# Kernel optimization log

Hardware: AMD Instinct MI355X
Metric: run time of the kernel (lower is better)

Reference implementation:

```python
import jax, jax.numpy as jnp
import numpy as np

N_ENT = 100000
N_REL = 500
IN_DIM = 128
OUT_DIM = 128
N_TRIP = 250000
BN_EPS = 1e-5
LRELU_SLOPE = 0.01


def setup_inputs() -> dict:
    key = jax.random.key(0)
    ks = jax.random.split(key, 10)
    heads = jax.random.randint(ks[0], (N_TRIP, 1), 0, N_ENT, dtype=jnp.int32)
    tails = jax.random.randint(ks[1], (N_TRIP, 1), 0, N_ENT, dtype=jnp.int32)
    rels = jax.random.randint(ks[2], (N_TRIP, 1), 0, N_REL, dtype=jnp.int32)
    triplets = jnp.concatenate([heads, tails, rels], axis=1)
    embed_range = (6.0 + 2.0) / OUT_DIM  # (margin + epsilon) / out_dim
    ent_embed = jax.random.uniform(ks[3], (N_ENT, IN_DIM), jnp.float32, -embed_range, embed_range)
    rel_embed = jax.random.uniform(ks[4], (N_REL, IN_DIM), jnp.float32, -embed_range, embed_range)
    a_w = jax.random.normal(ks[5], (OUT_DIM, 3 * IN_DIM), jnp.float32) * (1.414 * (2.0 / (3 * IN_DIM + OUT_DIM)) ** 0.5)
    a_b = jnp.zeros((OUT_DIM,), jnp.float32)
    a2_w = jax.random.normal(ks[6], (1, OUT_DIM), jnp.float32) * (1.414 * (2.0 / (OUT_DIM + 1)) ** 0.5)
    a2_b = jnp.zeros((1,), jnp.float32)
    return dict(
        triplets=triplets,
        ent_embed=ent_embed,
        rel_embed=rel_embed,
        a_w=a_w,
        a_b=a_b,
        a2_w=a2_w,
        a2_b=a2_b,
        bn0_g=jnp.ones((3 * IN_DIM,), jnp.float32),
        bn0_b=jnp.zeros((3 * IN_DIM,), jnp.float32),
        bn1_g=jnp.ones((OUT_DIM,), jnp.float32),
        bn1_b=jnp.zeros((OUT_DIM,), jnp.float32),
    )


def _batchnorm(x, gamma, beta):
    # training-mode BN: batch statistics over axis 0, biased variance
    mean = jnp.mean(x, axis=0)
    var = jnp.mean(jnp.square(x - mean), axis=0)
    return (x - mean) * jax.lax.rsqrt(var + BN_EPS) * gamma + beta


def _leaky_relu(x):
    return jnp.where(x >= 0, x, LRELU_SLOPE * x)


def reference(triplets, ent_embed, rel_embed, a_w, a_b, a2_w, a2_b,
              bn0_g, bn0_b, bn1_g, bn1_b):
    t0, t1, t2 = triplets[:, 0], triplets[:, 1], triplets[:, 2]
    e0 = ent_embed[t0]           # [n, in_dim]
    e1 = ent_embed[t1]           # [n, in_dim]
    r = rel_embed[t2]            # [n, in_dim]
    h_fwd = jnp.concatenate([e0, e1, r], axis=1)    # [n, 3*in_dim]
    h_bwd = jnp.concatenate([e1, e0, -r], axis=1)   # [n, 3*in_dim]
    h = jnp.concatenate([h_fwd, h_bwd], axis=0)     # [2n, 3*in_dim]
    h = _batchnorm(h, bn0_g, bn0_b)                 # dropout omitted (eval)
    c = _batchnorm(h @ a_w.T + a_b, bn1_g, bn1_b)   # [2n, out_dim]
    b = -_leaky_relu(c @ a2_w.T + a2_b)             # [2n, 1]
    e_b = jnp.exp(b)                                # [2n, 1]

    # edges[0] = cat(t0, t1); scatter-add messages into source node slots
    seg = jnp.concatenate([t0, t1], axis=0)         # [2n]
    temp1 = e_b * c                                 # [2n, out_dim]
    ebs = jax.ops.segment_sum(e_b, seg, num_segments=N_ENT)    # [N, 1]
    hs = jax.ops.segment_sum(temp1, seg, num_segments=N_ENT)   # [N, out_dim]
    ebs = jnp.where(ebs == 0, 1e-12, ebs)
    h_ent = hs / ebs                                # [N, out_dim]

    # scatter-mean of forward-direction messages by relation id
    rel_sum = jax.ops.segment_sum(temp1[:N_TRIP], t2, num_segments=N_REL)
    rel_cnt = jax.ops.segment_sum(jnp.ones((N_TRIP, 1), temp1.dtype), t2, num_segments=N_REL)
    h_rel = rel_sum / jnp.maximum(rel_cnt, 1.0)     # [R, out_dim]
    return h_ent, h_rel
```

## Files before the change

### kernel.cpp

```cpp
#include <hip/hip_runtime.h>
#include <hip/hip_bf16.h>

#define NE 100000
#define NR 500
#define DD 128
#define NT 250000
#define NEV 500000
#define RELOFF 12800000
#define TWO_NF 500000.0f
#define NTF 250000.0f
#define TBH 2048
#define NBH ((NT + TBH - 1)/TBH)
#define NBS ((NE + 1023)/1024)

typedef __attribute__((ext_vector_type(8))) short short8;
typedef __attribute__((ext_vector_type(4))) float f32x4;

__device__ __forceinline__ float bf2f(unsigned short u){
  unsigned int x = ((unsigned int)u) << 16;
  return __uint_as_float(x);
}
__device__ __forceinline__ float bf2f_lo(unsigned int u){ return __uint_as_float(u << 16); }
__device__ __forceinline__ float bf2f_hi(unsigned int u){ return __uint_as_float(u & 0xFFFF0000u); }
__device__ __forceinline__ unsigned short f2bf(float f){
  __hip_bfloat16 h = __float2bfloat16(f);
  return *reinterpret_cast<unsigned short*>(&h);
}
__device__ __forceinline__ void atomAddF(float* p, float v){ unsafeAtomicAdd(p, v); }
__device__ __forceinline__ float wredsum(float x){
  x += __shfl_xor(x, 1, 64);  x += __shfl_xor(x, 2, 64);  x += __shfl_xor(x, 4, 64);
  x += __shfl_xor(x, 8, 64);  x += __shfl_xor(x, 16, 64); x += __shfl_xor(x, 32, 64);
  return x;
}

__global__ __launch_bounds__(256) void k_hist(const int* __restrict__ trip,
                                              int* __restrict__ cnt, int* __restrict__ gHist){
  __shared__ int h[NR];
  int t = threadIdx.x;
  for (int r = t; r < NR; r += 256) h[r] = 0;
  __syncthreads();
  int b0 = blockIdx.x*TBH, b1 = min(b0+TBH, NT);
  for (int i = b0 + t; i < b1; i += 256){
    int t0 = trip[3*i], t1 = trip[3*i+1], t2 = trip[3*i+2];
    atomicAdd(&cnt[t0], 1);
    atomicAdd(&cnt[t1], 1);
    atomicAdd(&h[t2], 1);
  }
  __syncthreads();
  for (int r = t; r < NR; r += 256) gHist[blockIdx.x*NR + r] = h[r];
}

__global__ __launch_bounds__(512) void k_histscan(const int* __restrict__ gHist,
                                                  int* __restrict__ base, int* __restrict__ cntR,
                                                  int* __restrict__ offR){
  __shared__ int sm[512];
  int r = threadIdx.x;
  int s = 0;
  if (r < NR){
    for (int b = 0; b < NBH; ++b){ base[b*NR + r] = s; s += gHist[b*NR + r]; }
    cntR[r] = s;
  }
  sm[r] = (r < NR) ? s : 0;
  __syncthreads();
  for (int st = 1; st < 512; st <<= 1){
    int x = (r >= st) ? sm[r-st] : 0;
    __syncthreads();
    sm[r] += x;
    __syncthreads();
  }
  if (r < NR){
    int off = sm[r] - s;
    offR[r] = off;
    for (int b = 0; b < NBH; ++b) base[b*NR + r] += off;
  }
  if (r == 0) offR[NR] = NT;
}

__global__ __launch_bounds__(1024) void k_scan1(const int* __restrict__ cnt,
                                                int* __restrict__ off, int* __restrict__ bsum){
  __shared__ int wsum[16];
  int t = threadIdx.x, lane = t & 63, w = t >> 6;
  int i = blockIdx.x*1024 + t;
  int v = (i < NE) ? cnt[i] : 0;
  int x = v;
  #pragma unroll
  for (int s = 1; s < 64; s <<= 1){ int y = __shfl_up(x, s, 64); if (lane >= s) x += y; }
  if (lane == 63) wsum[w] = x;
  __syncthreads();
  if (w == 0 && lane < 16){
    int xs = wsum[lane];
    #pragma unroll
    for (int s = 1; s < 16; s <<= 1){ int y = __shfl_up(xs, s, 16); if ((lane & 15) >= s) xs += y; }
    wsum[lane] = xs;
  }
  __syncthreads();
  int wprev = (w == 0) ? 0 : wsum[w-1];
  int incl = wprev + x;
  if (i < NE) off[i] = incl - v;
  if (t == 1023) bsum[blockIdx.x] = incl;
}

__global__ __launch_bounds__(128) void k_scan2(const int* __restrict__ bsum,
                                               int* __restrict__ bbase, int* __restrict__ off){
  __shared__ int sm[128];
  int t = threadIdx.x;
  int v = (t < NBS) ? bsum[t] : 0;
  sm[t] = v; __syncthreads();
  for (int s = 1; s < 128; s <<= 1){
    int x = (t >= s) ? sm[t-s] : 0;
    __syncthreads();
    sm[t] += x;
    __syncthreads();
  }
  int incl = sm[t];
  if (t < NBS) bbase[t] = incl - v;
  if (t == NBS-1) off[NE] = incl;
}

__global__ __launch_bounds__(1024) void k_scan3(int* __restrict__ off, int* __restrict__ cur,
                                                const int* __restrict__ bbase){
  int i = blockIdx.x*1024 + threadIdx.x;
  if (i < NE){
    int o = off[i] + bbase[blockIdx.x];
    off[i] = o;
    cur[i] = o;
  }
}

__global__ void k_scat_ent(const int* __restrict__ trip, int* __restrict__ curE,
                           unsigned long long* __restrict__ evE){
  int i = blockIdx.x*blockDim.x + threadIdx.x;
  if (i < NT){
    int t0 = trip[3*i+0], t1 = trip[3*i+1], t2 = trip[3*i+2];
    int p0 = atomicAdd(&curE[t0], 1);
    unsigned long long e0 = (unsigned)t0 |
      ((unsigned long long)(((unsigned)t1 << 10) | ((unsigned)t2 << 1)) << 32);
    __builtin_nontemporal_store(e0, &evE[p0]);
    int p1 = atomicAdd(&curE[t1], 1);
    unsigned long long e1 = (unsigned)t1 |
      ((unsigned long long)(((unsigned)t0 << 10) | ((unsigned)t2 << 1) | 1u) << 32);
    __builtin_nontemporal_store(e1, &evE[p1]);
  }
}

__global__ __launch_bounds__(256) void k_scat_rel(const int* __restrict__ trip,
                                                  const int* __restrict__ base,
                                                  unsigned long long* __restrict__ evR){
  __shared__ int cur[NR];
  int t = threadIdx.x;
  for (int r = t; r < NR; r += 256) cur[r] = base[blockIdx.x*NR + r];
  __syncthreads();
  int b0 = blockIdx.x*TBH, b1 = min(b0+TBH, NT);
  for (int i = b0 + t; i < b1; i += 256){
    int t0 = trip[3*i], t1 = trip[3*i+1], t2 = trip[3*i+2];
    int p = atomicAdd(&cur[t2], 1);
    unsigned long long e = (unsigned)t0 | ((unsigned long long)(unsigned)t1 << 32);
    __builtin_nontemporal_store(e, &evR[p]);
  }
}

__global__ __launch_bounds__(256) void k_entstats(const float* __restrict__ ent, const int* __restrict__ cnt,
                                                  float* __restrict__ S, float* __restrict__ Q,
                                                  unsigned short* __restrict__ Xbf){
  int j = threadIdx.x & 127;
  int half = threadIdx.x >> 7;
  int r0 = blockIdx.x*128 + half;
  int r1 = min(blockIdx.x*128 + 128, NE);
  float s = 0.f, q = 0.f;
  for (int r = r0; r < r1; r += 2){
    float x = ent[(size_t)r*DD + j];
    Xbf[(size_t)r*DD + j] = f2bf(x);
    int w = cnt[r];
    if (w){
      float wf = (float)w;
      s += wf*x; q += wf*x*x;
    }
  }
  __shared__ float ss[256], qq[256];
  ss[threadIdx.x] = s; qq[threadIdx.x] = q; __syncthreads();
  if (half == 0){
    atomAddF(&S[j], ss[j] + ss[j+128]);
    atomAddF(&Q[j], qq[j] + qq[j+128]);
  }
}

__global__ void k_alpha(const float* __restrict__ rel, const int* __restrict__ cntR,
                        const float* __restrict__ S, const float* __restrict__ Q,
                        const float* __restrict__ bn0g, const float* __restrict__ bn0b,
                        float* __restrict__ alpha0, float* __restrict__ alpha1, float* __restrict__ alpha2,
                        float* __restrict__ beta0, float* __restrict__ beta1){
  int j = threadIdx.x;
  float qr = 0.f;
  for (int k = 0; k < NR; ++k){
    float w = (float)cntR[k];
    float x = rel[k*DD + j];
    qr += w*x*x;
  }
  float mean = S[j] / TWO_NF;
  float var  = Q[j] / TWO_NF - mean*mean;
  float inv  = rsqrtf(var + 1e-5f);
  float a0 = inv * bn0g[j];
  float a1 = inv * bn0g[128+j];
  alpha0[j] = a0; alpha1[j] = a1;
  beta0[j] = bn0b[j]     - mean*a0;
  beta1[j] = bn0b[128+j] - mean*a1;
  float varR = qr / NTF;
  alpha2[j] = rsqrtf(varR + 1e-5f) * bn0g[256+j];
}

__global__ void k_bias(const float* __restrict__ aw, const float* __restrict__ ab,
                       const float* __restrict__ bn0b,
                       const float* __restrict__ beta0, const float* __restrict__ beta1,
                       float* __restrict__ bias){
  int o = blockIdx.x, j = threadIdx.x;
  const float* r = aw + (size_t)o*384;
  float p = r[j]*beta0[j] + r[128+j]*beta1[j] + r[256+j]*bn0b[256+j];
  __shared__ float sm[128];
  sm[j] = p; __syncthreads();
  for (int s = 64; s > 0; s >>= 1){ if (j < s) sm[j] += sm[j+s]; __syncthreads(); }
  if (j == 0) bias[o] = ab[o] + sm[0];
}

__global__ void k_v(const float* __restrict__ rel, const float* __restrict__ aw,
                    const float* __restrict__ alpha2, float* __restrict__ V){
  int k = blockIdx.x, o = threadIdx.x;
  __shared__ float rl[128];
  rl[o] = rel[k*DD + o] * alpha2[o];
  __syncthreads();
  float acc = 0.f;
  #pragma unroll 8
  for (int j = 0; j < 128; ++j) acc += aw[(size_t)o*384 + 256 + j] * rl[j];
  V[k*DD + o] = acc;
}

__global__ void k_wfold2(const float* __restrict__ aw, const float* __restrict__ alpha0,
                         const float* __restrict__ alpha1, unsigned short* __restrict__ Wt2){
  int o = blockIdx.x;
  int k = threadIdx.x;
  float w;
  if (o < 128) w = aw[(size_t)o*384 + k] * alpha0[k];
  else         w = aw[(size_t)(o-128)*384 + 128 + k] * alpha1[k];
  Wt2[(size_t)o*128 + k] = f2bf(w);
}

__global__ __launch_bounds__(256) void k_u2(const unsigned short* __restrict__ Xbf,
                                            const unsigned short* __restrict__ Wt2,
                                            unsigned short* __restrict__ Uo){
  int tid = threadIdx.x;
  int w = tid >> 6, l = tid & 63;
  int col = l & 15, grp = l >> 4, kof = grp*8;
  int e0w = (blockIdx.x*4 + w)*16;
  int e = min(e0w + col, NE-1);
  const unsigned short* xrow = Xbf + (size_t)e*DD;
  short8 a0v = *(const short8*)(xrow + kof);
  short8 a1v = *(const short8*)(xrow + 32 + kof);
  short8 a2v = *(const short8*)(xrow + 64 + kof);
  short8 a3v = *(const short8*)(xrow + 96 + kof);

  f32x4 acc[16];
  #pragma unroll
  for (int ot = 0; ot < 16; ++ot) acc[ot] = (f32x4){0.f, 0.f, 0.f, 0.f};

  #pragma unroll
  for (int ot = 0; ot < 16; ++ot){
    const unsigned short* bbase = Wt2 + (size_t)(ot*16 + col)*128 + kof;
    short8 b0 = *(const short8*)(bbase);
    short8 b1 = *(const short8*)(bbase + 32);
    short8 b2 = *(const short8*)(bbase + 64);
    short8 b3 = *(const short8*)(bbase + 96);
    acc[ot] = __builtin_amdgcn_mfma_f32_16x16x32_bf16(a0v, b0, acc[ot], 0, 0, 0);
    acc[ot] = __builtin_amdgcn_mfma_f32_16x16x32_bf16(a1v, b1, acc[ot], 0, 0, 0);
    acc[ot] = __builtin_amdgcn_mfma_f32_16x16x32_bf16(a2v, b2, acc[ot], 0, 0, 0);
    acc[ot] = __builtin_amdgcn_mfma_f32_16x16x32_bf16(a3v, b3, acc[ot], 0, 0, 0);
  }

  #pragma unroll
  for (int ot = 0; ot < 16; ++ot){
    #pragma unroll
    for (int r = 0; r < 4; ++r){
      int row = e0w + 4*grp + r;
      if (row < NE)
        Uo[(size_t)row*256 + ot*16 + col] = f2bf(acc[ot][r]);
    }
  }
}

__global__ __launch_bounds__(256) void k_c1b(const uint2* __restrict__ evE,
                   const unsigned short* __restrict__ U, const float* __restrict__ V,
                   const float* __restrict__ bias,
                   float* __restrict__ colsum, float* __restrict__ colsumsq){
  int lane = threadIdx.x & 63;
  int w = threadIdx.x >> 6;
  int wv = blockIdx.x*4 + w;
  int nwv = gridDim.x*4;
  int per = (NEV + nwv - 1) / nwv;
  int st = wv*per, en = min(st + per, NEV);
  int c0 = 2*lane, c1 = c0+1;
  float b0 = bias[c0], b1 = bias[c1];
  const ushort2* Ub = (const ushort2*)U;
  const float2*  Vp = (const float2*)V;
  float s0=0.f, s1=0.f, q0=0.f, q1=0.f;
  for (int bs = st; bs < en; bs += 64){
    int n = min(64, en - bs);
    uint2 ev = (bs + lane < en) ? evE[bs + lane] : make_uint2(0u, 0u);
    int j = 0;
    for (; j + 4 <= n; j += 4){
      unsigned ow0 = __shfl(ev.x, j, 64),   pk0 = __shfl(ev.y, j, 64);
      unsigned ow1 = __shfl(ev.x, j+1, 64), pk1 = __shfl(ev.y, j+1, 64);
      unsigned ow2 = __shfl(ev.x, j+2, 64), pk2 = __shfl(ev.y, j+2, 64);
      unsigned ow3 = __shfl(ev.x, j+3, 64), pk3 = __shfl(ev.y, j+3, 64);
      ushort2 a0 = Ub[(size_t)ow0*128 + lane];
      ushort2 g0 = Ub[(size_t)(pk0 >> 10)*128 + 64 + lane];
      float2  v0 = Vp[((pk0 >> 1) & 0x1FF)*64 + lane];
      ushort2 a1 = Ub[(size_t)ow1*128 + lane];
      ushort2 g1 = Ub[(size_t)(pk1 >> 10)*128 + 64 + lane];
      float2  v1 = Vp[((pk1 >> 1) & 0x1FF)*64 + lane];
      ushort2 a2 = Ub[(size_t)ow2*128 + lane];
      ushort2 g2 = Ub[(size_t)(pk2 >> 10)*128 + 64 + lane];
      float2  v2 = Vp[((pk2 >> 1) & 0x1FF)*64 + lane];
      ushort2 a3 = Ub[(size_t)ow3*128 + lane];
      ushort2 g3 = Ub[(size_t)(pk3 >> 10)*128 + 64 + lane];
      float2  v3 = Vp[((pk3 >> 1) & 0x1FF)*64 + lane];
      float sg0 = (pk0 & 1) ? -1.f : 1.f;
      float sg1 = (pk1 & 1) ? -1.f : 1.f;
      float sg2 = (pk2 & 1) ? -1.f : 1.f;
      float sg3 = (pk3 & 1) ? -1.f : 1.f;
      float y00 = bf2f(a0.x) + bf2f(g0.x) + sg0*v0.x + b0;
      float y01 = bf2f(a0.y) + bf2f(g0.y) + sg0*v0.y + b1;
      float y10 = bf2f(a1.x) + bf2f(g1.x) + sg1*v1.x + b0;
      float y11 = bf2f(a1.y) + bf2f(g1.y) + sg1*v1.y + b1;
      float y20 = bf2f(a2.x) + bf2f(g2.x) + sg2*v2.x + b0;
      float y21 = bf2f(a2.y) + bf2f(g2.y) + sg2*v2.y + b1;
      float y30 = bf2f(a3.x) + bf2f(g3.x) + sg3*v3.x + b0;
      float y31 = bf2f(a3.y) + bf2f(g3.y) + sg3*v3.y + b1;
      s0 += y00 + y10 + y20 + y30;
      s1 += y01 + y11 + y21 + y31;
      q0 += y00*y00 + y10*y10 + y20*y20 + y30*y30;
      q1 += y01*y01 + y11*y11 + y21*y21 + y31*y31;
    }
    for (; j < n; ++j){
      unsigned ow0 = __shfl(ev.x, j, 64), pk0 = __shfl(ev.y, j, 64);
      ushort2 a0 = Ub[(size_t)ow0*128 + lane];
      ushort2 g0 = Ub[(size_t)(pk0 >> 10)*128 + 64 + lane];
      float2  v0 = Vp[((pk0 >> 1) & 0x1FF)*64 + lane];
      float sg0 = (pk0 & 1) ? -1.f : 1.f;
      float y00 = bf2f(a0.x) + bf2f(g0.x) + sg0*v0.x + b0;
      float y01 = bf2f(a0.y) + bf2f(g0.y) + sg0*v0.y + b1;
      s0 += y00;  q0 += y00*y00;
      s1 += y01;  q1 += y01*y01;
    }
  }
  __shared__ float sred[4][128], qred[4][128];
  sred[w][c0] = s0; sred[w][c1] = s1;
  qred[w][c0] = q0; qred[w][c1] = q1;
  __syncthreads();
  int t = threadIdx.x;
  if (t < 128){
    atomAddF(&colsum[t],   sred[0][t] + sred[1][t] + sred[2][t] + sred[3][t]);
    atomAddF(&colsumsq[t], qred[0][t] + qred[1][t] + qred[2][t] + qred[3][t]);
  }
}

__global__ void k_bn1fin(const float* __restrict__ colsum, const float* __restrict__ colsumsq,
                         const float* __restrict__ bn1g, const float* __restrict__ bn1b,
                         const float* __restrict__ a2w, const float* __restrict__ a2b,
                         const float* __restrict__ biasv,
                         float* __restrict__ A1, float* __restrict__ B1,
                         float* __restrict__ a2A, float* __restrict__ sbase){
  int j = threadIdx.x;
  float mean = colsum[j] / TWO_NF;
  float var  = colsumsq[j] / TWO_NF - mean*mean;
  float A = rsqrtf(var + 1e-5f) * bn1g[j];
  float B = bn1b[j] - mean*A;
  A1[j] = A; B1[j] = B;
  float w2 = a2w[j];
  float aA = w2*A;
  a2A[j] = aA;
  __shared__ float sm[128], sm2[128];
  sm[j] = w2*B; sm2[j] = biasv[j]*aA;
  __syncthreads();
  for (int s = 64; s > 0; s >>= 1){
    if (j < s){ sm[j] += sm[j+s]; sm2[j] += sm2[j+s]; }
    __syncthreads();
  }
  if (j == 0){
    float sb = a2b[0] + sm[0];
    sbase[0] = sb;
    sbase[1] = sb + sm2[0];
  }
}

__global__ __launch_bounds__(256) void k_sigma(const unsigned short* __restrict__ U,
                                               const float* __restrict__ a2A,
                                               float* __restrict__ sig){
  int lane = threadIdx.x & 63;
  int e = blockIdx.x*4 + (threadIdx.x>>6);
  if (e >= NE) return;
  const uint2* Ur = (const uint2*)U;
  uint2 r = Ur[(size_t)e*64 + lane];
  int c = (lane & 31)*4;
  float4 w = *(const float4*)&a2A[c];
  float p = bf2f_lo(r.x)*w.x + bf2f_hi(r.x)*w.y + bf2f_lo(r.y)*w.z + bf2f_hi(r.y)*w.w;
  p += __shfl_xor(p, 1, 64); p += __shfl_xor(p, 2, 64); p += __shfl_xor(p, 4, 64);
  p += __shfl_xor(p, 8, 64); p += __shfl_xor(p, 16, 64);
  if ((lane & 31) == 0) sig[2*e + (lane >> 5)] = p;
}

__global__ __launch_bounds__(256) void k_rho(const float* __restrict__ V,
                                             const float* __restrict__ a2A,
                                             float* __restrict__ rho){
  int lane = threadIdx.x & 63;
  int k = blockIdx.x*4 + (threadIdx.x>>6);
  if (k >= NR) return;
  const float2* Vp = (const float2*)V;
  float2 v = Vp[(size_t)k*64 + lane];
  int c0 = 2*lane;
  float p = v.x*a2A[c0] + v.y*a2A[c0+1];
  p = wredsum(p);
  if (lane == 0) rho[k] = p;
}

__global__ __launch_bounds__(256) void k_gent(const uint2* __restrict__ evE, const int* __restrict__ offE,
                   const unsigned short* __restrict__ U, const float* __restrict__ V,
                   const float* __restrict__ sig, const float* __restrict__ rho,
                   const float* __restrict__ bias,
                   const float* __restrict__ A1, const float* __restrict__ B1,
                   const float* __restrict__ sbase,
                   float* __restrict__ out){
  int lane = threadIdx.x & 63;
  int e = blockIdx.x*4 + (threadIdx.x>>6);
  if (e >= NE) return;
  int c0 = 2*lane, c1 = c0+1;
  const ushort2* Ub = (const ushort2*)U;
  const float2*  Vp = (const float2*)V;
  ushort2 u0 = Ub[(size_t)e*128 + lane];
  float base0 = bf2f(u0.x) + bias[c0], base1 = bf2f(u0.y) + bias[c1];
  float pb  = sbase[1];
  float s0e = sig[2*e];
  float accU0=0.f, accU1=0.f, accV0=0.f, accV1=0.f, sep=0.f;
  int p0 = offE[e], p1 = offE[e+1];
  for (int bs = p0; bs < p1; bs += 64){
    int n = min(64, p1 - bs);
    unsigned ev = 0u; float ebl = 0.f;
    if (bs + lane < p1){
      ev = evE[bs + lane].y;
      int oth = ev >> 10, rl = (ev >> 1) & 0x1FF;
      float sg = (ev & 1) ? -1.f : 1.f;
      float s = s0e + sig[2*oth + 1] + sg*rho[rl] + pb;
      float bb = (s >= 0.f) ? -s : -0.01f*s;
      ebl = expf(bb);
    }
    sep += ebl;
    int j = 0;
    for (; j + 4 <= n; j += 4){
      unsigned e0 = __shfl(ev, j, 64);
      unsigned e1 = __shfl(ev, j+1, 64);
      unsigned e2 = __shfl(ev, j+2, 64);
      unsigned e3 = __shfl(ev, j+3, 64);
      float eb0 = __shfl(ebl, j, 64);
      float eb1 = __shfl(ebl, j+1, 64);
      float eb2 = __shfl(ebl, j+2, 64);
      float eb3 = __shfl(ebl, j+3, 64);
      ushort2 g0 = Ub[(size_t)(e0 >> 10)*128 + 64 + lane];
      ushort2 g1 = Ub[(size_t)(e1 >> 10)*128 + 64 + lane];
      ushort2 g2 = Ub[(size_t)(e2 >> 10)*128 + 64 + lane];
      ushort2 g3 = Ub[(size_t)(e3 >> 10)*128 + 64 + lane];
      float2 v0 = Vp[((e0 >> 1) & 0x1FF)*64 + lane];
      float2 v1 = Vp[((e1 >> 1) & 0x1FF)*64 + lane];
      float2 v2 = Vp[((e2 >> 1) & 0x1FF)*64 + lane];
      float2 v3 = Vp[((e3 >> 1) & 0x1FF)*64 + lane];
      float w0 = (e0 & 1) ? -eb0 : eb0;
      float w1 = (e1 & 1) ? -eb1 : eb1;
      float w2 = (e2 & 1) ? -eb2 : eb2;
      float w3 = (e3 & 1) ? -eb3 : eb3;
      accU0 += eb0*bf2f(g0.x); accU1 += eb0*bf2f(g0.y);
      accV0 += w0*v0.x;        accV1 += w0*v0.y;
      accU0 += eb1*bf2f(g1.x); accU1 += eb1*bf2f(g1.y);
      accV0 += w1*v1.x;        accV1 += w1*v1.y;
      accU0 += eb2*bf2f(g2.x); accU1 += eb2*bf2f(g2.y);
      accV0 += w2*v2.x;        accV1 += w2*v2.y;
      accU0 += eb3*bf2f(g3.x); accU1 += eb3*bf2f(g3.y);
      accV0 += w3*v3.x;        accV1 += w3*v3.y;
    }
    for (; j < n; ++j){
      unsigned e0 = __shfl(ev, j, 64);
      float eb0 = __shfl(ebl, j, 64);
      ushort2 g0 = Ub[(size_t)(e0 >> 10)*128 + 64 + lane];
      float2 v0 = Vp[((e0 >> 1) & 0x1FF)*64 + lane];
      float w0 = (e0 & 1) ? -eb0 : eb0;
      accU0 += eb0*bf2f(g0.x); accU1 += eb0*bf2f(g0.y);
      accV0 += w0*v0.x;        accV1 += w0*v0.y;
    }
  }
  float se = wredsum(sep);
  float sY0 = se*base0 + accU0 + accV0;
  float sY1 = se*base1 + accU1 + accV1;
  float hs0 = A1[c0]*sY0 + B1[c0]*se;
  float hs1 = A1[c1]*sY1 + B1[c1]*se;
  float d = (se == 0.f) ? 1e-12f : se;
  out[(size_t)e*DD + c0] = hs0/d;
  out[(size_t)e*DD + c1] = hs1/d;
}

__global__ __launch_bounds__(256) void k_grel(const uint2* __restrict__ evR, const int* __restrict__ offR,
                   const unsigned short* __restrict__ U, const float* __restrict__ V,
                   const float* __restrict__ sig, const float* __restrict__ rho,
                   const float* __restrict__ bias,
                   const float* __restrict__ A1, const float* __restrict__ B1,
                   const float* __restrict__ sbase,
                   float* __restrict__ out){
  int lane = threadIdx.x & 63;
  int k = blockIdx.x >> 3;
  int wvs = (blockIdx.x & 7)*4 + (threadIdx.x >> 6);
  int c0 = 2*lane, c1 = c0+1;
  const ushort2* Ub = (const ushort2*)U;
  const float2*  Vp = (const float2*)V;
  float2 v = Vp[(size_t)k*64 + lane];
  float vb0 = v.x + bias[c0], vb1 = v.y + bias[c1];
  float rpb = rho[k] + sbase[1];
  float accY0=0.f, accY1=0.f, sep=0.f;
  int p0 = offR[k], p1 = offR[k+1];
  int tot = p1 - p0, per = (tot + 31) >> 5;
  int st = p0 + wvs*per, en = min(st + per, p1);
  for (int bs = st; bs < en; bs += 64){
    int n = min(64, en - bs);
    uint2 ev = make_uint2(0u, 0u); float ebl = 0.f;
    if (bs + lane < en){
      ev = evR[bs + lane];
      float s = sig[2*ev.x] + sig[2*ev.y + 1] + rpb;
      float bb = (s >= 0.f) ? -s : -0.01f*s;
      ebl = expf(bb);
    }
    sep += ebl;
    int j = 0;
    for (; j + 2 <= n; j += 2){
      unsigned a0 = __shfl(ev.x, j, 64),   d0 = __shfl(ev.y, j, 64);
      unsigned a1 = __shfl(ev.x, j+1, 64), d1 = __shfl(ev.y, j+1, 64);
      float eb0 = __shfl(ebl, j, 64);
      float eb1 = __shfl(ebl, j+1, 64);
      ushort2 ua0 = Ub[(size_t)a0*128 + lane];
      ushort2 ud0 = Ub[(size_t)d0*128 + 64 + lane];
      ushort2 ua1 = Ub[(size_t)a1*128 + lane];
      ushort2 ud1 = Ub[(size_t)d1*128 + 64 + lane];
      accY0 += eb0*(bf2f(ua0.x) + bf2f(ud0.x));
      accY1 += eb0*(bf2f(ua0.y) + bf2f(ud0.y));
      accY0 += eb1*(bf2f(ua1.x) + bf2f(ud1.x));
      accY1 += eb1*(bf2f(ua1.y) + bf2f(ud1.y));
    }
    for (; j < n; ++j){
      unsigned a0 = __shfl(ev.x, j, 64), d0 = __shfl(ev.y, j, 64);
      float eb0 = __shfl(ebl, j, 64);
      ushort2 ua0 = Ub[(size_t)a0*128 + lane];
      ushort2 ud0 = Ub[(size_t)d0*128 + 64 + lane];
      accY0 += eb0*(bf2f(ua0.x) + bf2f(ud0.x));
      accY1 += eb0*(bf2f(ua0.y) + bf2f(ud0.y));
    }
  }
  float se = wredsum(sep);
  float sY0 = accY0 + se*vb0;
  float sY1 = accY1 + se*vb1;
  float r0 = A1[c0]*sY0 + B1[c0]*se;
  float r1 = A1[c1]*sY1 + B1[c1]*se;
  atomAddF(&out[(size_t)RELOFF + (size_t)k*DD + c0], r0);
  atomAddF(&out[(size_t)RELOFF + (size_t)k*DD + c1], r1);
}

__global__ void k_fin_rel(float* __restrict__ out, const int* __restrict__ cntR){
  int idx = blockIdx.x*blockDim.x + threadIdx.x;
  int k = idx >> 7;
  float c = fmaxf((float)cntR[k], 1.f);
  out[RELOFF + idx] = out[RELOFF + idx] / c;
}

extern "C" void kernel_launch(void* const* d_in, const int* in_sizes, int n_in,
                              void* d_out, int out_size, void* d_ws, size_t ws_size,
                              hipStream_t stream) {
  (void)in_sizes; (void)n_in; (void)ws_size; (void)out_size;
  const int*   trip = (const int*)  d_in[0];
  const float* ent  = (const float*)d_in[1];
  const float* rel  = (const float*)d_in[2];
  const float* aw   = (const float*)d_in[3];
  const float* ab   = (const float*)d_in[4];
  const float* a2w  = (const float*)d_in[5];
  const float* a2b  = (const float*)d_in[6];
  const float* bn0g = (const float*)d_in[7];
  const float* bn0b = (const float*)d_in[8];
  const float* bn1g = (const float*)d_in[9];
  const float* bn1b = (const float*)d_in[10];
  float* out = (float*)d_out;
  unsigned short* Xbf = (unsigned short*)d_out;

  char* w = (char*)d_ws;
  size_t off = 0;
  auto take = [&](size_t bytes) -> char* {
    char* p = w + off;
    off = (off + bytes + 511) & ~(size_t)511;
    return p;
  };
  float* S        = (float*)take(512);
  float* Q        = (float*)take(512);
  float* colsum   = (float*)take(512);
  float* colsumsq = (float*)take(512);
  int*   cnt      = (int*)  take((size_t)NE*4);
  size_t zero_end = off;
  int*   cntR   = (int*)  take((size_t)NR*4);
  float* alpha0 = (float*)take(512);
  float* alpha1 = (float*)take(512);
  float* alpha2 = (float*)take(512);
  float* beta0  = (float*)take(512);
  float* beta1  = (float*)take(512);
  float* biasv  = (float*)take(512);
  float* A1     = (float*)take(512);
  float* B1     = (float*)take(512);
  float* a2A    = (float*)take(512);
  float* sbase  = (float*)take(512);
  float* rho    = (float*)take((size_t)NR*4);
  float* sig    = (float*)take((size_t)NE*2*4);
  int*   offE   = (int*)  take((size_t)(NE+1)*4);
  int*   curE   = (int*)  take((size_t)NE*4);
  int*   offR   = (int*)  take((size_t)(NR+1)*4);
  int*   gHist  = (int*)  take((size_t)NBH*NR*4);
  int*   gBase  = (int*)  take((size_t)NBH*NR*4);
  int*   bsum   = (int*)  take((size_t)NBS*4);
  int*   bbase  = (int*)  take((size_t)NBS*4);
  unsigned long long* evE = (unsigned long long*)take((size_t)NEV*8);
  unsigned long long* evR = (unsigned long long*)take((size_t)NT*8);
  float* V      = (float*)take((size_t)NR*DD*4);
  unsigned short* Wt2 = (unsigned short*)take((size_t)256*128*2);
  unsigned short* U   = (unsigned short*)take((size_t)NE*256*2);

  hipMemsetAsync((char*)d_out + (size_t)RELOFF*4, 0, (size_t)NR*DD*4, stream);
  hipMemsetAsync(d_ws, 0, zero_end, stream);

  k_hist     <<<NBH, 256, 0, stream>>>(trip, cnt, gHist);
  k_histscan <<<1, 512, 0, stream>>>(gHist, gBase, cntR, offR);
  k_scan1    <<<NBS, 1024, 0, stream>>>(cnt, offE, bsum);
  k_scan2    <<<1, 128, 0, stream>>>(bsum, bbase, offE);
  k_scan3    <<<NBS, 1024, 0, stream>>>(offE, curE, bbase);
  k_scat_ent <<<(NT+255)/256, 256, 0, stream>>>(trip, curE, evE);
  k_scat_rel <<<NBH, 256, 0, stream>>>(trip, gBase, evR);
  k_entstats <<<(NE+127)/128, 256, 0, stream>>>(ent, cnt, S, Q, Xbf);
  k_alpha    <<<1, 128, 0, stream>>>(rel, cntR, S, Q, bn0g, bn0b, alpha0, alpha1, alpha2, beta0, beta1);
  k_bias     <<<128, 128, 0, stream>>>(aw, ab, bn0b, beta0, beta1, biasv);
  k_v        <<<NR, 128, 0, stream>>>(rel, aw, alpha2, V);
  k_wfold2   <<<256, 128, 0, stream>>>(aw, alpha0, alpha1, Wt2);
  k_u2       <<<1563, 256, 0, stream>>>(Xbf, Wt2, U);
  k_c1b      <<<2048, 256, 0, stream>>>((const uint2*)evE, U, V, biasv, colsum, colsumsq);
  k_bn1fin   <<<1, 128, 0, stream>>>(colsum, colsumsq, bn1g, bn1b, a2w, a2b, biasv, A1, B1, a2A, sbase);
  k_sigma    <<<NE/4, 256, 0, stream>>>(U, a2A, sig);
  k_rho      <<<(NR+3)/4, 256, 0, stream>>>(V, a2A, rho);
  k_gent     <<<NE/4, 256, 0, stream>>>((const uint2*)evE, offE, U, V, sig, rho, biasv, A1, B1, sbase, out);
  k_grel     <<<NR*8, 256, 0, stream>>>((const uint2*)evR, offR, U, V, sig, rho, biasv, A1, B1, sbase, out);
  k_fin_rel  <<<(NR*DD)/256, 256, 0, stream>>>(out, cntR);
}
```

Measured before the change: 403.9 us.

## Restructure k_u2 so each wave keeps a weight slice in registers

In the entity projection GEMM kernel, work is now split so each wave owns 4 output tiles and holds those weight fragments in registers. It then loops over 4 entity tiles of 16 rows, instead of each wave loading all 16 weight tiles for one 16-row entity tile. This cuts redundant weight loads per block and the 16-accumulator register footprint, which may raise occupancy. In exchange, each wave now loads entity rows four times per block and has a longer serial chain of MFMA and store per iteration.

```diff
diff --git a/kernel.cpp b/kernel.cpp
--- a/kernel.cpp
+++ b/kernel.cpp
@@ -249,38 +249,69 @@
   int tid = threadIdx.x;
   int w = tid >> 6, l = tid & 63;
   int col = l & 15, grp = l >> 4, kof = grp*8;
-  int e0w = (blockIdx.x*4 + w)*16;
-  int e = min(e0w + col, NE-1);
-  const unsigned short* xrow = Xbf + (size_t)e*DD;
-  short8 a0v = *(const short8*)(xrow + kof);
-  short8 a1v = *(const short8*)(xrow + 32 + kof);
-  short8 a2v = *(const short8*)(xrow + 64 + kof);
-  short8 a3v = *(const short8*)(xrow + 96 + kof);
-
-  f32x4 acc[16];
+  int e0 = blockIdx.x*64;
+  int ot0 = w*4;
+
+  const unsigned short* wb0 = Wt2 + (size_t)((ot0+0)*16 + col)*128 + kof;
+  const unsigned short* wb1 = Wt2 + (size_t)((ot0+1)*16 + col)*128 + kof;
+  const unsigned short* wb2 = Wt2 + (size_t)((ot0+2)*16 + col)*128 + kof;
+  const unsigned short* wb3 = Wt2 + (size_t)((ot0+3)*16 + col)*128 + kof;
+  short8 b00 = *(const short8*)(wb0);
+  short8 b01 = *(const short8*)(wb0+32);
+  short8 b02 = *(const short8*)(wb0+64);
+  short8 b03 = *(const short8*)(wb0+96);
+  short8 b10 = *(const short8*)(wb1);
+  short8 b11 = *(const short8*)(wb1+32);
+  short8 b12 = *(const short8*)(wb1+64);
+  short8 b13 = *(const short8*)(wb1+96);
+  short8 b20 = *(const short8*)(wb2);
+  short8 b21 = *(const short8*)(wb2+32);
+  short8 b22 = *(const short8*)(wb2+64);
+  short8 b23 = *(const short8*)(wb2+96);
+  short8 b30 = *(const short8*)(wb3);
+  short8 b31 = *(const short8*)(wb3+32);
+  short8 b32 = *(const short8*)(wb3+64);
+  short8 b33 = *(const short8*)(wb3+96);
+
   #pragma unroll
-  for (int ot = 0; ot < 16; ++ot) acc[ot] = (f32x4){0.f, 0.f, 0.f, 0.f};
-
-  #pragma unroll
-  for (int ot = 0; ot < 16; ++ot){
-    const unsigned short* bbase = Wt2 + (size_t)(ot*16 + col)*128 + kof;
-    short8 b0 = *(const short8*)(bbase);
-    short8 b1 = *(const short8*)(bbase + 32);
-    short8 b2 = *(const short8*)(bbase + 64);
-    short8 b3 = *(const short8*)(bbase + 96);
-    acc[ot] = __builtin_amdgcn_mfma_f32_16x16x32_bf16(a0v, b0, acc[ot], 0, 0, 0);
-    acc[ot] = __builtin_amdgcn_mfma_f32_16x16x32_bf16(a1v, b1, acc[ot], 0, 0, 0);
-    acc[ot] = __builtin_amdgcn_mfma_f32_16x16x32_bf16(a2v, b2, acc[ot], 0, 0, 0);
-    acc[ot] = __builtin_amdgcn_mfma_f32_16x16x32_bf16(a3v, b3, acc[ot], 0, 0, 0);
-  }
-
-  #pragma unroll
-  for (int ot = 0; ot < 16; ++ot){
+  for (int et = 0; et < 4; ++et){
+    int ebase = e0 + et*16;
+    int e = min(ebase + col, NE-1);
+    const unsigned short* xrow = Xbf + (size_t)e*DD;
+    short8 a0 = *(const short8*)(xrow + kof);
+    short8 a1 = *(const short8*)(xrow + 32 + kof);
+    short8 a2 = *(const short8*)(xrow + 64 + kof);
+    short8 a3 = *(const short8*)(xrow + 96 + kof);
+    f32x4 c0 = (f32x4){0.f,0.f,0.f,0.f};
+    f32x4 c1 = (f32x4){0.f,0.f,0.f,0.f};
+    f32x4 c2 = (f32x4){0.f,0.f,0.f,0.f};
+    f32x4 c3 = (f32x4){0.f,0.f,0.f,0.f};
+    c0 = __builtin_amdgcn_mfma_f32_16x16x32_bf16(a0, b00, c0, 0, 0, 0);
+    c1 = __builtin_amdgcn_mfma_f32_16x16x32_bf16(a0, b10, c1, 0, 0, 0);
+    c2 = __builtin_amdgcn_mfma_f32_16x16x32_bf16(a0, b20, c2, 0, 0, 0);
+    c3 = __builtin_amdgcn_mfma_f32_16x16x32_bf16(a0, b30, c3, 0, 0, 0);
+    c0 = __builtin_amdgcn_mfma_f32_16x16x32_bf16(a1, b01, c0, 0, 0, 0);
+    c1 = __builtin_amdgcn_mfma_f32_16x16x32_bf16(a1, b11, c1, 0, 0, 0);
+    c2 = __builtin_amdgcn_mfma_f32_16x16x32_bf16(a1, b21, c2, 0, 0, 0);
+    c3 = __builtin_amdgcn_mfma_f32_16x16x32_bf16(a1, b31, c3, 0, 0, 0);
+    c0 = __builtin_amdgcn_mfma_f32_16x16x32_bf16(a2, b02, c0, 0, 0, 0);
+    c1 = __builtin_amdgcn_mfma_f32_16x16x32_bf16(a2, b12, c1, 0, 0, 0);
+    c2 = __builtin_amdgcn_mfma_f32_16x16x32_bf16(a2, b22, c2, 0, 0, 0);
+    c3 = __builtin_amdgcn_mfma_f32_16x16x32_bf16(a2, b32, c3, 0, 0, 0);
+    c0 = __builtin_amdgcn_mfma_f32_16x16x32_bf16(a3, b03, c0, 0, 0, 0);
+    c1 = __builtin_amdgcn_mfma_f32_16x16x32_bf16(a3, b13, c1, 0, 0, 0);
+    c2 = __builtin_amdgcn_mfma_f32_16x16x32_bf16(a3, b23, c2, 0, 0, 0);
+    c3 = __builtin_amdgcn_mfma_f32_16x16x32_bf16(a3, b33, c3, 0, 0, 0);
     #pragma unroll
     for (int r = 0; r < 4; ++r){
-      int row = e0w + 4*grp + r;
-      if (row < NE)
-        Uo[(size_t)row*256 + ot*16 + col] = f2bf(acc[ot][r]);
+      int row = ebase + 4*grp + r;
+      if (row < NE){
+        size_t rb = (size_t)row*256 + col;
+        Uo[rb + (ot0+0)*16] = f2bf(c0[r]);
+        Uo[rb + (ot0+1)*16] = f2bf(c1[r]);
+        Uo[rb + (ot0+2)*16] = f2bf(c2[r]);
+        Uo[rb + (ot0+3)*16] = f2bf(c3[r]);
+      }
     }
   }
 }
```

New measurement: 375.9 us. 1.07x faster.
